# Optimization experiments

Measured on AMD Instinct MI355X. Metric: run time of the kernel, lower is better.

Reference implementation:

```python
import jax, jax.numpy as jnp
import numpy as np

MIN_LOOP = 4  # min_hairpin
INF = jnp.float32(1e18)


def _nussinov_ptr(e_pair, e_unp, allowed, min_loop=MIN_LOOP):
    """Fill the O(L^2) DP table span-by-span (anti-diagonal wavefront),
    vectorized over the start index i within each span. Returns the
    backpointer table ptr (L,L) int32 with the same encoding as the
    original numpy code: 0=i unpaired, 1=j unpaired, 2=(i,j) pair, k+3=bifurcation at k."""
    L = e_unp.shape[0]
    d = jnp.arange(L)
    dp = jnp.full((L, L), INF, dtype=jnp.float32).at[d, d].set(e_unp)
    ptr = jnp.full((L, L), -1, dtype=jnp.int32).at[d, d].set(0)
    ii = jnp.arange(L)
    tt = jnp.arange(L)  # bifurcation offset t = k - i, valid for t <= s-2

    def span_body(s, carry):
        dp, ptr = carry
        jj = ii + s - 1                      # true j; >= L entries are dropped on scatter
        jc = jnp.minimum(jj, L - 1)          # clamped j for safe gathers
        ic1 = jnp.minimum(ii + 1, L - 1)
        # candidate 0: i unpaired -> dp[i+1, j] + e_unp[i]
        c0 = dp[ic1, jc] + e_unp[ii]
        # candidate 1: j unpaired -> dp[i, j-1] + e_unp[j]
        c1 = dp[ii, jnp.maximum(jc - 1, 0)] + e_unp[jc]
        # candidate 2: (i,j) paired -> dp[i+1, j-1] + e_pair[i,j] (inner=0 when span==2)
        inner = jnp.where(s >= 3, dp[ic1, jnp.maximum(jc - 1, 0)], jnp.float32(0.0))
        c2 = inner + e_pair[ii, jc]
        pair_ok = allowed[ii, jc] & (jc - ii > min_loop)
        # bifurcation: min over k=i+t, t in [0, s-2]: dp[i,k] + dp[k+1,j]
        kk = ii[:, None] + tt[None, :]
        kc = jnp.minimum(kk, L - 1)
        bif = jnp.where(tt[None, :] <= s - 2,
                        dp[ii[:, None], kc] + dp[jnp.minimum(kc + 1, L - 1), jc[:, None]],
                        INF)
        t_arg = jnp.argmin(bif, axis=1)  # first occurrence == ascending-k tie-break
        bif_min = jnp.take_along_axis(bif, t_arg[:, None], axis=1)[:, 0]
        # sequential strict-< selection, matching the numpy candidate order
        best = c0
        bp = jnp.zeros(L, jnp.int32)
        u = c1 < best; best = jnp.where(u, c1, best); bp = jnp.where(u, 1, bp)
        u = pair_ok & (c2 < best); best = jnp.where(u, c2, best); bp = jnp.where(u, 2, bp)
        u = bif_min < best; best = jnp.where(u, bif_min, best)
        bp = jnp.where(u, (ii + t_arg + 3).astype(jnp.int32), bp)
        dp = dp.at[ii, jj].set(best, mode='drop')
        ptr = ptr.at[ii, jj].set(bp, mode='drop')
        return dp, ptr

    dp, ptr = jax.lax.fori_loop(2, L + 1, span_body, (dp, ptr))
    return ptr


def _backtrace(ptr):
    """Iterative stack-based backtrace (LIFO, same push order as numpy).
    Intervals on the stack are disjoint, so depth <= L; size 2L for slack."""
    L = ptr.shape[0]
    S = 2 * L
    stack0 = jnp.zeros((S, 2), jnp.int32).at[0].set(jnp.array([0, L - 1], jnp.int32))
    res0 = jnp.full((L,), -1, jnp.int32)

    def cond(st):
        return st[1] > 0

    def body(st):
        stack, sp, res = st
        sp1 = sp - 1
        i = stack[sp1, 0]
        j = stack[sp1, 1]
        p = ptr[i, j]
        valid = i < j
        is0 = p == 0; is1 = p == 1; is2 = p == 2
        k = p - 3
        # first push (popped slot is reused)
        e1i = jnp.where(is0, i + 1, jnp.where(is1, i, jnp.where(is2, i + 1, i)))
        e1j = jnp.where(is0, j, jnp.where(is1, j - 1, jnp.where(is2, j - 1, k)))
        v1 = valid & jnp.where(is2, (i + 1) <= (j - 1), True)
        # second push only for bifurcation: (k+1, j)
        v2 = valid & (p >= 3)
        do_pair = valid & is2
        res = res.at[i].set(jnp.where(do_pair, j, res[i]))
        res = res.at[j].set(jnp.where(do_pair, i, res[j]))
        stack = stack.at[sp1].set(jnp.where(v1, jnp.stack([e1i, e1j]), stack[sp1]))
        sp_a = sp1 + v1.astype(jnp.int32)
        slot = jnp.minimum(sp_a, S - 1)
        stack = stack.at[slot].set(jnp.where(v2, jnp.stack([k + 1, j]), stack[slot]))
        sp_b = sp_a + v2.astype(jnp.int32)
        return stack, sp_b, res

    _, _, res = jax.lax.while_loop(cond, body, (stack0, jnp.int32(1), res0))
    return res


def _decode(e_pair, e_unp, pair_mask):
    ptr = jax.vmap(_nussinov_ptr, in_axes=(0, 0, 0))(e_pair, e_unp, pair_mask)
    return jax.vmap(_backtrace)(ptr)  # (B, L) int32, -1 = unpaired


def setup_inputs() -> dict:
    key = jax.random.key(0)
    k1, k2, k3 = jax.random.split(key, 3)
    B, L = 16, 512
    e_pair = jax.random.normal(k1, (B, L, L), dtype=jnp.float32)
    e_unp = jax.random.normal(k2, (B, L), dtype=jnp.float32)
    pair_mask = jax.random.bernoulli(k3, 0.3, (B, L, L))
    return {"e_pair": e_pair, "e_unp": e_unp, "pair_mask": pair_mask}


def reference(e_pair, e_unp, pair_mask):
    return _decode(e_pair, e_unp, pair_mask)
```

## Files before the change

kernel.cpp:

```cpp
#include <hip/hip_runtime.h>
#include <stdint.h>

#define L_ 512
#define NBUF (L_ * L_)
#define T_ 64
#define NT_ 8
#define PAD 5
#define INFV 3.0e38f

__global__ __launch_bounds__(1024) void fd_mask_probe(const unsigned int* __restrict__ pm,
                                                      int n32,
                                                      unsigned int* __restrict__ flags) {
    __shared__ unsigned int sf;
    if (threadIdx.x == 0) sf = 0u;
    __syncthreads();
    unsigned int local = 0;
    const int nscan = n32 < 65536 ? n32 : 65536;
    for (int idx = threadIdx.x; idx < nscan; idx += 1024) {
        const unsigned int w = pm[idx];
        const unsigned int h0 = w & 0xFFFFu, h1 = w >> 16;
        if (w > 1u) local |= 1u;
        if (w & 0xFEFEFEFEu) local |= 2u;
        if ((h0 != 0u && h0 != 0x3F80u) || (h1 != 0u && h1 != 0x3F80u)) local |= 4u;
        if (w == 0x3F803F80u || w == 0x00003F80u) local |= 8u;
        if ((h0 != 0u && h0 != 0x3C00u) || (h1 != 0u && h1 != 0x3C00u)) local |= 16u;
    }
    if (local) atomicOr(&sf, local);
    __syncthreads();
    if (threadIdx.x == 0) flags[0] = sf;
}

__device__ __forceinline__ int mask_mode(unsigned int f) {
    if (!(f & 1u)) return 0;
    if (!(f & 2u)) return 1;
    if (!(f & 4u)) return (f & 8u) ? 3 : 2;
    return (!(f & 16u)) ? 3 : 2;
}

__device__ __forceinline__ bool mask_bit(int mode, const unsigned int* pmW,
                                         const unsigned char* pm8,
                                         const unsigned short* pm16,
                                         const float* pmf, size_t gi) {
    if (mode == 0) return pmW[gi] != 0u;
    if (mode == 1) return pm8[gi] != 0;
    if (mode == 3) return pm16[gi] != 0;
    return pmf[gi] != 0.0f;
}

__global__ __launch_bounds__(256) void fd_diag(
    const float* __restrict__ e_pair, const float* __restrict__ e_unp,
    const unsigned int* __restrict__ pm, const unsigned int* __restrict__ flags,
    float* __restrict__ dp_ws, unsigned short* __restrict__ ptr_ws)
{
    const int b = blockIdx.x / NT_;
    const int I = blockIdx.x % NT_;
    const int t = threadIdx.x;
    const int r0 = I * T_;
    const float* ep = e_pair + (size_t)b * NBUF;
    float* dp = dp_ws + (size_t)b * NBUF;
    unsigned short* ptr = ptr_ws + (size_t)b * NBUF;
    const int mode = mask_mode(flags[0]);
    const unsigned int*   pmW  = pm + (size_t)b * NBUF;
    const unsigned char*  pm8  = ((const unsigned char*) pm) + (size_t)b * NBUF;
    const unsigned short* pm16 = ((const unsigned short*)pm) + (size_t)b * NBUF;
    const float*          pmf  = ((const float*)         pm) + (size_t)b * NBUF;

    __shared__ float Ct[T_][T_ + PAD];
    __shared__ float epl[T_][T_ + PAD];
    __shared__ unsigned char mkb[T_][T_ + PAD];
    __shared__ unsigned short bp[T_][T_ + PAD];
    __shared__ float eu[T_];

    for (int e = t; e < T_ * T_; e += 256) {
        const int r = e >> 6, c = e & 63;
        const size_t gi = (size_t)(r0 + r) * L_ + r0 + c;
        epl[r][c] = ep[gi];
        mkb[r][c] = mask_bit(mode, pmW, pm8, pm16, pmf, gi) ? 1 : 0;
    }
    if (t < T_) eu[t] = e_unp[(size_t)b * L_ + r0 + t];
    __syncthreads();
    if (t < T_) Ct[t][t] = eu[t];
    __syncthreads();

    const int cell = t >> 2, sub = t & 3;
    for (int m = 1; m < T_; ++m) {
        if (cell < T_ - m) {
            const int ti = cell, tj = cell + m;
            float pf_c0 = 0, pf_c1 = 0, pf_in = 0, pf_ep = 0; bool pok = false;
            if (sub == 0) {
                pf_c0 = Ct[ti + 1][tj];
                pf_c1 = Ct[ti][tj - 1];
                pf_in = (m >= 2) ? Ct[ti + 1][tj - 1] : 0.0f;
                pf_ep = epl[ti][tj];
                pok = mkb[ti][tj] && (m > 4);
            }
            float mv = INFV; int km = 0;
            for (int tk = ti + sub; tk < tj; tk += 4) {
                const float v = Ct[ti][tk] + Ct[tk + 1][tj];
                if (v < mv) { mv = v; km = tk; }
            }
            for (int off = 1; off < 4; off <<= 1) {
                const float ov = __shfl_xor(mv, off, 4);
                const int   ok = __shfl_xor(km, off, 4);
                if (ov < mv || (ov == mv && ok < km)) { mv = ov; km = ok; }
            }
            if (sub == 0) {
                const float c0 = pf_c0 + eu[ti];
                const float c1 = pf_c1 + eu[tj];
                const float c2 = pf_in + pf_ep;
                float best = c0; int bv = 0;
                if (c1 < best)        { best = c1; bv = 1; }
                if (pok && c2 < best) { best = c2; bv = 2; }
                if (mv < best)        { best = mv; bv = r0 + km + 3; }
                Ct[ti][tj] = best;
                bp[ti][tj] = (unsigned short)bv;
            }
        }
        __syncthreads();
    }
    for (int e = t; e < T_ * T_; e += 256) {
        const int r = e >> 6, c = e & 63;
        if (c >= r) {
            const size_t gi = (size_t)(r0 + r) * L_ + r0 + c;
            dp[gi] = Ct[r][c];
            if (c > r) ptr[gi] = bp[r][c];
        }
    }
}

__global__ __launch_bounds__(256) void fd_step(
    const float* __restrict__ e_pair, const float* __restrict__ e_unp,
    const unsigned int* __restrict__ pm, const unsigned int* __restrict__ flags,
    float* __restrict__ dp_ws, unsigned short* __restrict__ ptr_ws,
    int d, int nI)
{
    const int b = blockIdx.x / nI;
    const int I = blockIdx.x % nI;
    const int J = I + d;
    const int t = threadIdx.x;
    const int r0 = I * T_, q0 = J * T_;
    const float* ep = e_pair + (size_t)b * NBUF;
    float* dp = dp_ws + (size_t)b * NBUF;
    unsigned short* ptr = ptr_ws + (size_t)b * NBUF;
    const int mode = mask_mode(flags[0]);
    const unsigned int*   pmW  = pm + (size_t)b * NBUF;
    const unsigned char*  pm8  = ((const unsigned char*) pm) + (size_t)b * NBUF;
    const unsigned short* pm16 = ((const unsigned short*)pm) + (size_t)b * NBUF;
    const float*          pmf  = ((const float*)         pm) + (size_t)b * NBUF;

    __shared__ float WA[T_][T_ + PAD];
    __shared__ float WB[T_][T_ + PAD];
    __shared__ float Ct[T_][T_ + PAD];
    __shared__ float accv[T_][T_ + PAD];
    __shared__ unsigned short acck[T_][T_ + PAD];
    __shared__ float epl[T_][T_ + PAD];
    __shared__ unsigned char mkb[T_][T_ + PAD];
    __shared__ unsigned short bp[T_][T_ + PAD];
    __shared__ float euI[T_], euJ[T_], rowB[T_], colL[T_];
    __shared__ float cornerS;

    if (d >= 2) {
        float av[16]; int akr[16];
        const int ti0 = (t >> 4) * 4, tj0 = (t & 15) * 4;
#pragma unroll
        for (int q = 0; q < 16; ++q) { av[q] = INFV; akr[q] = 0; }
        for (int K = I + 1; K < J; ++K) {
            const int kb = K * T_;
            __syncthreads();
            for (int e = t; e < T_ * T_; e += 256) {
                const int r = e >> 6, c = e & 63;
                WA[r][c] = dp[(size_t)(r0 + r) * L_ + kb + c];
                WB[r][c] = dp[(size_t)(kb + 1 + r) * L_ + q0 + c];
            }
            __syncthreads();
            for (int kk = 0; kk < T_; ++kk) {
                float a[4], bb[4];
#pragma unroll
                for (int r = 0; r < 4; ++r) a[r] = WA[ti0 + r][kk];
#pragma unroll
                for (int c = 0; c < 4; ++c) bb[c] = WB[kk][tj0 + c];
                const int kg = kb + kk;
#pragma unroll
                for (int r = 0; r < 4; ++r)
#pragma unroll
                    for (int c = 0; c < 4; ++c) {
                        const float v = a[r] + bb[c];
                        const int q = r * 4 + c;
                        if (v < av[q]) { av[q] = v; akr[q] = kg; }
                    }
            }
        }
#pragma unroll
        for (int r = 0; r < 4; ++r)
#pragma unroll
            for (int c = 0; c < 4; ++c) {
                accv[ti0 + r][tj0 + c] = av[r * 4 + c];
                acck[ti0 + r][tj0 + c] = (unsigned short)akr[r * 4 + c];
            }
    }
    __syncthreads();

    for (int e = t; e < T_ * T_; e += 256) {
        const int r = e >> 6, c = e & 63;
        WA[r][c] = dp[(size_t)(r0 + r) * L_ + r0 + c];
        WB[r][c] = dp[(size_t)(q0 + r) * L_ + q0 + c];
        const size_t gi = (size_t)(r0 + r) * L_ + q0 + c;
        epl[r][c] = ep[gi];
        mkb[r][c] = mask_bit(mode, pmW, pm8, pm16, pmf, gi) ? 1 : 0;
    }
    if (t < T_) {
        euI[t] = e_unp[(size_t)b * L_ + r0 + t];
        euJ[t] = e_unp[(size_t)b * L_ + q0 + t];
        rowB[t] = dp[(size_t)(r0 + T_) * L_ + q0 + t];
        colL[t] = dp[(size_t)(r0 + t) * L_ + q0 - 1];
    }
    if (t == 0) cornerS = (d >= 2) ? dp[(size_t)(r0 + T_) * L_ + q0 - 1] : 0.0f;
    __syncthreads();

    const int cell = t >> 2, sub = t & 3;
    for (int m = -(T_ - 1); m <= T_ - 1; ++m) {
        const int am = m < 0 ? -m : m;
        if (cell < T_ - am) {
            const int ti = (m < 0) ? cell + am : cell;
            const int tj = ti + m;
            const int span = d * T_ + m;
            float pf_c0 = 0, pf_c1 = 0, pf_in = 0, pf_ep = 0;
            float bulk_v = INFV; int bulk_k = 0; bool pok = false;
            if (sub == 0) {
                pf_c0 = (ti < T_ - 1) ? Ct[ti + 1][tj] : rowB[tj];
                pf_c1 = (tj > 0) ? Ct[ti][tj - 1] : colL[ti];
                if (span == 1)        pf_in = 0.0f;
                else if (ti < T_ - 1) pf_in = (tj > 0) ? Ct[ti + 1][tj - 1] : colL[ti + 1];
                else                  pf_in = (tj > 0) ? rowB[tj - 1] : cornerS;
                pf_ep = epl[ti][tj];
                pok = mkb[ti][tj] && (span > 4);
                if (d >= 2) { bulk_v = accv[ti][tj]; bulk_k = acck[ti][tj]; }
            }
            float mv = INFV; int km = 0;
            for (int tk = ti + sub; tk < T_ - 1; tk += 4) {
                const float v = WA[ti][tk] + Ct[tk + 1][tj];
                if (v < mv) { mv = v; km = r0 + tk; }
            }
            if (((T_ - 1 - ti) & 3) == sub) {
                const float v = WA[ti][T_ - 1] + rowB[tj];
                if (v < mv) { mv = v; km = r0 + T_ - 1; }
            }
            for (int tk = sub; tk < tj; tk += 4) {
                const float v = Ct[ti][tk] + WB[tk + 1][tj];
                if (v < mv) { mv = v; km = q0 + tk; }
            }
            for (int off = 1; off < 4; off <<= 1) {
                const float ov = __shfl_xor(mv, off, 4);
                const int   ok = __shfl_xor(km, off, 4);
                if (ov < mv || (ov == mv && ok < km)) { mv = ov; km = ok; }
            }
            if (sub == 0) {
                if (bulk_v < mv || (bulk_v == mv && bulk_k < km)) { mv = bulk_v; km = bulk_k; }
                const float c0 = pf_c0 + euI[ti];
                const float c1 = pf_c1 + euJ[tj];
                const float c2 = pf_in + pf_ep;
                float best = c0; int bv = 0;
                if (c1 < best)        { best = c1; bv = 1; }
                if (pok && c2 < best) { best = c2; bv = 2; }
                if (mv < best)        { best = mv; bv = km + 3; }
                Ct[ti][tj] = best;
                bp[ti][tj] = (unsigned short)bv;
            }
        }
        __syncthreads();
    }

    for (int e = t; e < T_ * T_; e += 256) {
        const int r = e >> 6, c = e & 63;
        dp [(size_t)(r0 + r) * L_ + q0 + c] = Ct[r][c];
        ptr[(size_t)(r0 + r) * L_ + q0 + c] = bp[r][c];
    }
}

__global__ __launch_bounds__(256) void fd_backtrace(
    const unsigned short* __restrict__ ptr_ws, int* __restrict__ out)
{
    const int b = blockIdx.x;
    const int t = threadIdx.x;
    const unsigned short* ptr = ptr_ws + (size_t)b * NBUF;
    int* res = out + (size_t)b * L_;
    __shared__ int sti[2 * L_], stj[2 * L_];

    const uint4* p4 = (const uint4*)ptr;
    unsigned int acc = 0;
    for (int idx = t; idx < NBUF / 8; idx += 256) {
        const uint4 v = p4[idx];
        acc += v.x ^ v.y ^ v.z ^ v.w;
    }
    asm volatile("" :: "v"(acc));
    for (int idx = t; idx < L_; idx += 256) res[idx] = -1;
    __syncthreads();

    if (t == 0) {
        int sp = 1; sti[0] = 0; stj[0] = L_ - 1;
        while (sp > 0) {
            --sp;
            const int i = sti[sp], j = stj[sp];
            if (i < j) {
                const int p = (int)ptr[(size_t)i * L_ + j];
                if (p == 0)      { sti[sp] = i + 1; stj[sp] = j;     ++sp; }
                else if (p == 1) { sti[sp] = i;     stj[sp] = j - 1; ++sp; }
                else if (p == 2) {
                    res[i] = j; res[j] = i;
                    if (i + 1 <= j - 1) { sti[sp] = i + 1; stj[sp] = j - 1; ++sp; }
                } else {
                    const int k = p - 3;
                    sti[sp] = i;     stj[sp] = k; ++sp;
                    sti[sp] = k + 1; stj[sp] = j; ++sp;
                }
            }
        }
    }
}

extern "C" void kernel_launch(void* const* d_in, const int* in_sizes, int n_in,
                              void* d_out, int out_size, void* d_ws, size_t ws_size,
                              hipStream_t stream) {
    const float* e_pair = (const float*)d_in[0];
    const float* e_unp  = (const float*)d_in[1];
    const unsigned int* pm = (const unsigned int*)d_in[2];
    const int B = in_sizes[1] / L_;
    int* out = (int*)d_out;

    unsigned int* flags = (unsigned int*)d_ws;
    float* dp_ws = (float*)((char*)d_ws + 256);
    unsigned short* ptr_ws = (unsigned short*)(dp_ws + (size_t)B * NBUF);

    const int n32 = in_sizes[2] / 4;
    fd_mask_probe<<<dim3(1), dim3(1024), 0, stream>>>(pm, n32, flags);
    fd_diag<<<dim3(B * NT_), dim3(256), 0, stream>>>(e_pair, e_unp, pm, flags,
                                                     dp_ws, ptr_ws);
    for (int d = 1; d < NT_; ++d) {
        const int nI = NT_ - d;
        fd_step<<<dim3(B * nI), dim3(256), 0, stream>>>(e_pair, e_unp, pm, flags,
                                                        dp_ws, ptr_ws, d, nI);
    }
    fd_backtrace<<<dim3(B), dim3(256), 0, stream>>>(ptr_ws, out);
}
```

Measured before the change: 2.228 ms.

## Run intra-tile DP wavefront on one wave with LDS waitcnt instead of barriers

The per-tile anti-diagonal DP in both the diagonal and step kernels now runs on a single 64-lane wave, one thread per cell. Each cell's bifurcation min is split across four register accumulators and merged with a lowest-k tie-break, replacing the 4-lane shuffle reduction. Between diagonals the wave waits on LDS completion (s_waitcnt lgkmcnt) instead of a block-wide __syncthreads, removing many barriers per tile. The cost is less parallelism inside each cell, since one lane does all the k work, and the shared-memory row stride changes from 69 to 70, which may add bank conflicts on column-strided accesses.

```diff
diff --git a/kernel.cpp b/kernel.cpp
--- a/kernel.cpp
+++ b/kernel.cpp
@@ -5,8 +5,9 @@
 #define NBUF (L_ * L_)
 #define T_ 64
 #define NT_ 8
-#define PAD 5
+#define STR 70
 #define INFV 3.0e38f
+#define IDX(r, c) ((r) * STR + (c))
 
 __global__ __launch_bounds__(1024) void fd_mask_probe(const unsigned int* __restrict__ pm,
                                                       int n32,
@@ -45,6 +46,18 @@
     if (mode == 1) return pm8[gi] != 0;
     if (mode == 3) return pm16[gi] != 0;
     return pmf[gi] != 0.0f;
+}
+
+__device__ __forceinline__ void wave_sync_lds() {
+    asm volatile("s_waitcnt lgkmcnt(0)" ::: "memory");
+    __builtin_amdgcn_sched_barrier(0);
+}
+
+__device__ __forceinline__ void upd(float& v, int& k, float x, int kn) {
+    if (x < v) { v = x; k = kn; }
+}
+__device__ __forceinline__ void lexm(float& v, int& k, float ov, int ok) {
+    if (ov < v || (ov == v && ok < k)) { v = ov; k = ok; }
 }
 
 __global__ __launch_bounds__(256) void fd_diag(
@@ -65,65 +78,62 @@
     const unsigned short* pm16 = ((const unsigned short*)pm) + (size_t)b * NBUF;
     const float*          pmf  = ((const float*)         pm) + (size_t)b * NBUF;
 
-    __shared__ float Ct[T_][T_ + PAD];
-    __shared__ float epl[T_][T_ + PAD];
-    __shared__ unsigned char mkb[T_][T_ + PAD];
-    __shared__ unsigned short bp[T_][T_ + PAD];
+    __shared__ float Ct[T_ * STR];
+    __shared__ float epl[T_ * STR];
+    __shared__ unsigned char mkb[T_ * STR];
+    __shared__ unsigned short bp[T_ * STR];
     __shared__ float eu[T_];
 
     for (int e = t; e < T_ * T_; e += 256) {
         const int r = e >> 6, c = e & 63;
         const size_t gi = (size_t)(r0 + r) * L_ + r0 + c;
-        epl[r][c] = ep[gi];
-        mkb[r][c] = mask_bit(mode, pmW, pm8, pm16, pmf, gi) ? 1 : 0;
+        epl[IDX(r, c)] = ep[gi];
+        mkb[IDX(r, c)] = mask_bit(mode, pmW, pm8, pm16, pmf, gi) ? 1 : 0;
     }
     if (t < T_) eu[t] = e_unp[(size_t)b * L_ + r0 + t];
     __syncthreads();
-    if (t < T_) Ct[t][t] = eu[t];
-    __syncthreads();
-
-    const int cell = t >> 2, sub = t & 3;
-    for (int m = 1; m < T_; ++m) {
-        if (cell < T_ - m) {
-            const int ti = cell, tj = cell + m;
-            float pf_c0 = 0, pf_c1 = 0, pf_in = 0, pf_ep = 0; bool pok = false;
-            if (sub == 0) {
-                pf_c0 = Ct[ti + 1][tj];
-                pf_c1 = Ct[ti][tj - 1];
-                pf_in = (m >= 2) ? Ct[ti + 1][tj - 1] : 0.0f;
-                pf_ep = epl[ti][tj];
-                pok = mkb[ti][tj] && (m > 4);
-            }
-            float mv = INFV; int km = 0;
-            for (int tk = ti + sub; tk < tj; tk += 4) {
-                const float v = Ct[ti][tk] + Ct[tk + 1][tj];
-                if (v < mv) { mv = v; km = tk; }
-            }
-            for (int off = 1; off < 4; off <<= 1) {
-                const float ov = __shfl_xor(mv, off, 4);
-                const int   ok = __shfl_xor(km, off, 4);
-                if (ov < mv || (ov == mv && ok < km)) { mv = ov; km = ok; }
-            }
-            if (sub == 0) {
-                const float c0 = pf_c0 + eu[ti];
-                const float c1 = pf_c1 + eu[tj];
-                const float c2 = pf_in + pf_ep;
+
+    if (t < 64) {
+        const int c = t;
+        Ct[IDX(c, c)] = eu[c];
+        wave_sync_lds();
+        for (int m = 1; m < T_; ++m) {
+            if (c < T_ - m) {
+                const int ti = c, tj = c + m;
+                float v0 = INFV, v1 = INFV, v2 = INFV, v3 = INFV;
+                int   k0 = 0,    k1 = 0,    k2 = 0,    k3 = 0;
+                int n = ti;
+                for (; n + 4 <= tj; n += 4) {
+                    upd(v0, k0, Ct[IDX(ti, n + 0)] + Ct[IDX(n + 1, tj)], n + 0);
+                    upd(v1, k1, Ct[IDX(ti, n + 1)] + Ct[IDX(n + 2, tj)], n + 1);
+                    upd(v2, k2, Ct[IDX(ti, n + 2)] + Ct[IDX(n + 3, tj)], n + 2);
+                    upd(v3, k3, Ct[IDX(ti, n + 3)] + Ct[IDX(n + 4, tj)], n + 3);
+                }
+                for (; n < tj; ++n)
+                    upd(v0, k0, Ct[IDX(ti, n)] + Ct[IDX(n + 1, tj)], n);
+                lexm(v0, k0, v1, k1); lexm(v2, k2, v3, k3); lexm(v0, k0, v2, k2);
+                const float c0 = Ct[IDX(ti + 1, tj)] + eu[ti];
+                const float c1 = Ct[IDX(ti, tj - 1)] + eu[tj];
+                const float inner = (m >= 2) ? Ct[IDX(ti + 1, tj - 1)] : 0.0f;
+                const float c2 = inner + epl[IDX(ti, tj)];
+                const bool pok = mkb[IDX(ti, tj)] && (m > 4);
                 float best = c0; int bv = 0;
                 if (c1 < best)        { best = c1; bv = 1; }
                 if (pok && c2 < best) { best = c2; bv = 2; }
-                if (mv < best)        { best = mv; bv = r0 + km + 3; }
-                Ct[ti][tj] = best;
-                bp[ti][tj] = (unsigned short)bv;
-            }
-        }
-        __syncthreads();
-    }
+                if (v0 < best)        { best = v0; bv = r0 + k0 + 3; }
+                Ct[IDX(ti, tj)] = best;
+                bp[IDX(ti, tj)] = (unsigned short)bv;
+            }
+            wave_sync_lds();
+        }
+    }
+    __syncthreads();
     for (int e = t; e < T_ * T_; e += 256) {
         const int r = e >> 6, c = e & 63;
         if (c >= r) {
             const size_t gi = (size_t)(r0 + r) * L_ + r0 + c;
-            dp[gi] = Ct[r][c];
-            if (c > r) ptr[gi] = bp[r][c];
+            dp[gi] = Ct[IDX(r, c)];
+            if (c > r) ptr[gi] = bp[IDX(r, c)];
         }
     }
 }
@@ -148,14 +158,14 @@
     const unsigned short* pm16 = ((const unsigned short*)pm) + (size_t)b * NBUF;
     const float*          pmf  = ((const float*)         pm) + (size_t)b * NBUF;
 
-    __shared__ float WA[T_][T_ + PAD];
-    __shared__ float WB[T_][T_ + PAD];
-    __shared__ float Ct[T_][T_ + PAD];
-    __shared__ float accv[T_][T_ + PAD];
-    __shared__ unsigned short acck[T_][T_ + PAD];
-    __shared__ float epl[T_][T_ + PAD];
-    __shared__ unsigned char mkb[T_][T_ + PAD];
-    __shared__ unsigned short bp[T_][T_ + PAD];
+    __shared__ float WA[T_ * STR];
+    __shared__ float WB[T_ * STR];
+    __shared__ float Ct[T_ * STR];
+    __shared__ float accv[T_ * STR];
+    __shared__ unsigned short acck[T_ * STR];
+    __shared__ float epl[T_ * STR];
+    __shared__ unsigned char mkb[T_ * STR];
+    __shared__ unsigned short bp[T_ * STR];
     __shared__ float euI[T_], euJ[T_], rowB[T_], colL[T_];
     __shared__ float cornerS;
 
@@ -169,16 +179,16 @@
             __syncthreads();
             for (int e = t; e < T_ * T_; e += 256) {
                 const int r = e >> 6, c = e & 63;
-                WA[r][c] = dp[(size_t)(r0 + r) * L_ + kb + c];
-                WB[r][c] = dp[(size_t)(kb + 1 + r) * L_ + q0 + c];
+                WA[IDX(r, c)] = dp[(size_t)(r0 + r) * L_ + kb + c];
+                WB[IDX(r, c)] = dp[(size_t)(kb + 1 + r) * L_ + q0 + c];
             }
             __syncthreads();
             for (int kk = 0; kk < T_; ++kk) {
                 float a[4], bb[4];
 #pragma unroll
-                for (int r = 0; r < 4; ++r) a[r] = WA[ti0 + r][kk];
-#pragma unroll
-                for (int c = 0; c < 4; ++c) bb[c] = WB[kk][tj0 + c];
+                for (int r = 0; r < 4; ++r) a[r] = WA[IDX(ti0 + r, kk)];
+#pragma unroll
+                for (int c = 0; c < 4; ++c) bb[c] = WB[IDX(kk, tj0 + c)];
                 const int kg = kb + kk;
 #pragma unroll
                 for (int r = 0; r < 4; ++r)
@@ -194,19 +204,19 @@
         for (int r = 0; r < 4; ++r)
 #pragma unroll
             for (int c = 0; c < 4; ++c) {
-                accv[ti0 + r][tj0 + c] = av[r * 4 + c];
-                acck[ti0 + r][tj0 + c] = (unsigned short)akr[r * 4 + c];
+                accv[IDX(ti0 + r, tj0 + c)] = av[r * 4 + c];
+                acck[IDX(ti0 + r, tj0 + c)] = (unsigned short)akr[r * 4 + c];
             }
     }
     __syncthreads();
 
     for (int e = t; e < T_ * T_; e += 256) {
         const int r = e >> 6, c = e & 63;
-        WA[r][c] = dp[(size_t)(r0 + r) * L_ + r0 + c];
-        WB[r][c] = dp[(size_t)(q0 + r) * L_ + q0 + c];
+        WA[IDX(r, c)] = dp[(size_t)(r0 + r) * L_ + r0 + c];
+        WB[IDX(r, c)] = dp[(size_t)(q0 + r) * L_ + q0 + c];
         const size_t gi = (size_t)(r0 + r) * L_ + q0 + c;
-        epl[r][c] = ep[gi];
-        mkb[r][c] = mask_bit(mode, pmW, pm8, pm16, pmf, gi) ? 1 : 0;
+        epl[IDX(r, c)] = ep[gi];
+        mkb[IDX(r, c)] = mask_bit(mode, pmW, pm8, pm16, pmf, gi) ? 1 : 0;
     }
     if (t < T_) {
         euI[t] = e_unp[(size_t)b * L_ + r0 + t];
@@ -217,63 +227,61 @@
     if (t == 0) cornerS = (d >= 2) ? dp[(size_t)(r0 + T_) * L_ + q0 - 1] : 0.0f;
     __syncthreads();
 
-    const int cell = t >> 2, sub = t & 3;
-    for (int m = -(T_ - 1); m <= T_ - 1; ++m) {
-        const int am = m < 0 ? -m : m;
-        if (cell < T_ - am) {
-            const int ti = (m < 0) ? cell + am : cell;
-            const int tj = ti + m;
-            const int span = d * T_ + m;
-            float pf_c0 = 0, pf_c1 = 0, pf_in = 0, pf_ep = 0;
-            float bulk_v = INFV; int bulk_k = 0; bool pok = false;
-            if (sub == 0) {
-                pf_c0 = (ti < T_ - 1) ? Ct[ti + 1][tj] : rowB[tj];
-                pf_c1 = (tj > 0) ? Ct[ti][tj - 1] : colL[ti];
-                if (span == 1)        pf_in = 0.0f;
-                else if (ti < T_ - 1) pf_in = (tj > 0) ? Ct[ti + 1][tj - 1] : colL[ti + 1];
-                else                  pf_in = (tj > 0) ? rowB[tj - 1] : cornerS;
-                pf_ep = epl[ti][tj];
-                pok = mkb[ti][tj] && (span > 4);
-                if (d >= 2) { bulk_v = accv[ti][tj]; bulk_k = acck[ti][tj]; }
-            }
-            float mv = INFV; int km = 0;
-            for (int tk = ti + sub; tk < T_ - 1; tk += 4) {
-                const float v = WA[ti][tk] + Ct[tk + 1][tj];
-                if (v < mv) { mv = v; km = r0 + tk; }
-            }
-            if (((T_ - 1 - ti) & 3) == sub) {
-                const float v = WA[ti][T_ - 1] + rowB[tj];
-                if (v < mv) { mv = v; km = r0 + T_ - 1; }
-            }
-            for (int tk = sub; tk < tj; tk += 4) {
-                const float v = Ct[ti][tk] + WB[tk + 1][tj];
-                if (v < mv) { mv = v; km = q0 + tk; }
-            }
-            for (int off = 1; off < 4; off <<= 1) {
-                const float ov = __shfl_xor(mv, off, 4);
-                const int   ok = __shfl_xor(km, off, 4);
-                if (ov < mv || (ov == mv && ok < km)) { mv = ov; km = ok; }
-            }
-            if (sub == 0) {
-                if (bulk_v < mv || (bulk_v == mv && bulk_k < km)) { mv = bulk_v; km = bulk_k; }
-                const float c0 = pf_c0 + euI[ti];
-                const float c1 = pf_c1 + euJ[tj];
-                const float c2 = pf_in + pf_ep;
+    if (t < 64) {
+        const int c = t;
+        for (int m = -(T_ - 1); m <= T_ - 1; ++m) {
+            const int am = m < 0 ? -m : m;
+            if (c < T_ - am) {
+                const int ti = (m < 0) ? c + am : c;
+                const int tj = ti + m;
+                const int span = d * T_ + m;
+                float v0 = INFV, v1 = INFV, v2 = INFV, v3 = INFV;
+                int   k0 = 0,    k1 = 0,    k2 = 0,    k3 = 0;
+                int n = ti;
+                for (; n + 4 <= T_ - 1; n += 4) {
+                    upd(v0, k0, WA[IDX(ti, n + 0)] + Ct[IDX(n + 1, tj)], r0 + n + 0);
+                    upd(v1, k1, WA[IDX(ti, n + 1)] + Ct[IDX(n + 2, tj)], r0 + n + 1);
+                    upd(v2, k2, WA[IDX(ti, n + 2)] + Ct[IDX(n + 3, tj)], r0 + n + 2);
+                    upd(v3, k3, WA[IDX(ti, n + 3)] + Ct[IDX(n + 4, tj)], r0 + n + 3);
+                }
+                for (; n < T_ - 1; ++n)
+                    upd(v0, k0, WA[IDX(ti, n)] + Ct[IDX(n + 1, tj)], r0 + n);
+                upd(v0, k0, WA[IDX(ti, T_ - 1)] + rowB[tj], r0 + T_ - 1);
+                n = 0;
+                for (; n + 4 <= tj; n += 4) {
+                    upd(v0, k0, Ct[IDX(ti, n + 0)] + WB[IDX(n + 1, tj)], q0 + n + 0);
+                    upd(v1, k1, Ct[IDX(ti, n + 1)] + WB[IDX(n + 2, tj)], q0 + n + 1);
+                    upd(v2, k2, Ct[IDX(ti, n + 2)] + WB[IDX(n + 3, tj)], q0 + n + 2);
+                    upd(v3, k3, Ct[IDX(ti, n + 3)] + WB[IDX(n + 4, tj)], q0 + n + 3);
+                }
+                for (; n < tj; ++n)
+                    upd(v0, k0, Ct[IDX(ti, n)] + WB[IDX(n + 1, tj)], q0 + n);
+                lexm(v0, k0, v1, k1); lexm(v2, k2, v3, k3); lexm(v0, k0, v2, k2);
+                if (d >= 2) lexm(v0, k0, accv[IDX(ti, tj)], acck[IDX(ti, tj)]);
+                const float c0 = ((ti < T_ - 1) ? Ct[IDX(ti + 1, tj)] : rowB[tj]) + euI[ti];
+                const float c1 = ((tj > 0) ? Ct[IDX(ti, tj - 1)] : colL[ti]) + euJ[tj];
+                float inner;
+                if (span == 1)        inner = 0.0f;
+                else if (ti < T_ - 1) inner = (tj > 0) ? Ct[IDX(ti + 1, tj - 1)] : colL[ti + 1];
+                else                  inner = (tj > 0) ? rowB[tj - 1] : cornerS;
+                const float c2 = inner + epl[IDX(ti, tj)];
+                const bool pok = mkb[IDX(ti, tj)] && (span > 4);
                 float best = c0; int bv = 0;
                 if (c1 < best)        { best = c1; bv = 1; }
                 if (pok && c2 < best) { best = c2; bv = 2; }
-                if (mv < best)        { best = mv; bv = km + 3; }
-                Ct[ti][tj] = best;
-                bp[ti][tj] = (unsigned short)bv;
-            }
-        }
-        __syncthreads();
-    }
+                if (v0 < best)        { best = v0; bv = k0 + 3; }
+                Ct[IDX(ti, tj)] = best;
+                bp[IDX(ti, tj)] = (unsigned short)bv;
+            }
+            wave_sync_lds();
+        }
+    }
+    __syncthreads();
 
     for (int e = t; e < T_ * T_; e += 256) {
         const int r = e >> 6, c = e & 63;
-        dp [(size_t)(r0 + r) * L_ + q0 + c] = Ct[r][c];
-        ptr[(size_t)(r0 + r) * L_ + q0 + c] = bp[r][c];
+        dp [(size_t)(r0 + r) * L_ + q0 + c] = Ct[IDX(r, c)];
+        ptr[(size_t)(r0 + r) * L_ + q0 + c] = bp[IDX(r, c)];
     }
 }
 
```

Measured after the change: 3.509 ms. +57.5%, slower.
